# Kernel tuning notes

Hardware: AMD Instinct MI355X
Metric: run time of the kernel (lower is better)

Reference implementation:

```python
import jax, jax.numpy as jnp
import numpy as np

LN_EPS = 1e-5


def _layer_norm(x, scale, bias):
    mu = jnp.mean(x, axis=-1, keepdims=True)
    var = jnp.mean(jnp.square(x - mu), axis=-1, keepdims=True)
    return (x - mu) * jax.lax.rsqrt(var + LN_EPS) * scale + bias


def setup_inputs() -> dict:
    key = jax.random.key(0)
    B, N, C_Z, C_H = 1, 512, 128, 128
    ks = jax.random.split(key, 8)
    s = 1.0 / np.sqrt(C_Z)
    inp = {
        "z": jax.random.normal(ks[0], (B, N, N, C_Z), dtype=jnp.float32),
        "mask": jnp.ones((B, N, N), dtype=jnp.float32),
        # gated / plain projections from c_z -> c_hidden
        "w_a_p": jax.random.normal(ks[1], (C_Z, C_H), dtype=jnp.float32) * s,
        "b_a_p": jnp.zeros((C_H,), dtype=jnp.float32),
        "w_a_g": jnp.zeros((C_Z, C_H), dtype=jnp.float32),  # gating init: zeros, bias ones
        "b_a_g": jnp.ones((C_H,), dtype=jnp.float32),
        "w_b_p": jax.random.normal(ks[2], (C_Z, C_H), dtype=jnp.float32) * s,
        "b_b_p": jnp.zeros((C_H,), dtype=jnp.float32),
        "w_b_g": jnp.zeros((C_Z, C_H), dtype=jnp.float32),
        "b_b_g": jnp.ones((C_H,), dtype=jnp.float32),
        # output gate c_z -> c_z (gating init)
        "w_g": jnp.zeros((C_Z, C_Z), dtype=jnp.float32),
        "b_g": jnp.ones((C_Z,), dtype=jnp.float32),
        # final projection c_hidden -> c_z ('final' init: zeros; use small randn for a nontrivial test)
        "w_z": jax.random.normal(ks[3], (C_H, C_Z), dtype=jnp.float32) * (1.0 / np.sqrt(C_H)),
        "b_z": jnp.zeros((C_Z,), dtype=jnp.float32),
        "ln_in_scale": jnp.ones((C_Z,), dtype=jnp.float32),
        "ln_in_bias": jnp.zeros((C_Z,), dtype=jnp.float32),
        "ln_out_scale": jnp.ones((C_H,), dtype=jnp.float32),
        "ln_out_bias": jnp.zeros((C_H,), dtype=jnp.float32),
    }
    return inp


def reference(z, mask, w_a_p, b_a_p, w_a_g, b_a_g, w_b_p, b_b_p, w_b_g, b_b_g,
              w_g, b_g, w_z, b_z, ln_in_scale, ln_in_bias, ln_out_scale, ln_out_bias):
    # tmu_type == 'outgoing'
    z = _layer_norm(z, ln_in_scale, ln_in_bias)          # [B,N,N,Cz]
    m = mask[..., None]                                   # [B,N,N,1]
    a = jax.nn.sigmoid(z @ w_a_g + b_a_g) * m * (z @ w_a_p + b_a_p)  # [B,N,N,Ch]
    b = jax.nn.sigmoid(z @ w_b_g + b_b_g) * m * (z @ w_b_p + b_b_p)  # [B,N,N,Ch]
    # outgoing: p[b,i,j,c] = sum_k a[b,i,k,c] * b[b,j,k,c]
    x = jnp.einsum("bikc,bjkc->bijc", a, b)              # [B,N,N,Ch]
    x = _layer_norm(x, ln_out_scale, ln_out_bias)
    x = x @ w_z + b_z                                    # [B,N,N,Cz]
    g = jax.nn.sigmoid(z @ w_g + b_g)                    # [B,N,N,Cz]
    return x * g
```

## Files before the change

### kernel.cpp

```cpp
#include <hip/hip_runtime.h>

typedef __attribute__((ext_vector_type(8))) short short8;
typedef __attribute__((ext_vector_type(4))) short short4v;
typedef __attribute__((ext_vector_type(4))) float float4v;

#define NDIM 512
#define NN (NDIM*NDIM)
#define CD 128

__device__ __forceinline__ unsigned short f2b(float f) {
  union { float f; unsigned u; } v; v.f = f;
  unsigned r = v.u + 0x7FFFu + ((v.u >> 16) & 1u);
  return (unsigned short)(r >> 16);
}
__device__ __forceinline__ float b2f(unsigned short h) {
  union { unsigned u; float f; } v; v.u = ((unsigned)h) << 16; return v.f;
}
__device__ __forceinline__ float sigmoidf_(float x) {
  return __fdividef(1.f, 1.f + __expf(-x));
}
__device__ __forceinline__ unsigned pk2(float a, float b) {
  unsigned r;
  asm("v_cvt_pk_bf16_f32 %0, %1, %2" : "=v"(r) : "v"(a), "v"(b));
  return r;
}
__device__ __forceinline__ float4v mfma16(short8 a, short8 b, float4v c) {
  return __builtin_amdgcn_mfma_f32_16x16x32_bf16(a, b, c, 0, 0, 0);
}
__device__ __forceinline__ void gl_lds16(const short* g, short* l) {
  __builtin_amdgcn_global_load_lds(
      (const __attribute__((address_space(1))) unsigned int*)g,
      (__attribute__((address_space(3))) unsigned int*)l, 16, 0, 0);
}

__device__ __forceinline__ short8 fragr(const short* buf, int row, int j) {
  return *(const short8*)(buf + row * 128 + ((j ^ (row & 15)) << 3));
}
__device__ __forceinline__ void stg_w(short* buf, int row, int ku, unsigned v) {
  *(unsigned*)&buf[row * 128 + ((((ku >> 2) ^ (row & 15)) << 3) + ((ku & 3) << 1))] = v;
}
__device__ __forceinline__ void stg_w2(short* buf, int row, int ku, unsigned v0, unsigned v1) {
  unsigned long long v = (unsigned long long)v0 | ((unsigned long long)v1 << 32);
  *(unsigned long long*)&buf[row * 128 + ((((ku >> 2) ^ (row & 15)) << 3) + ((ku & 3) << 1))] = v;
}

__global__ __launch_bounds__(256) void kPrepW(
    const float* __restrict__ w0, const float* __restrict__ w1,
    const float* __restrict__ w2, const float* __restrict__ w3,
    const float* __restrict__ w4, short* __restrict__ wt)
{
  const int wi = blockIdx.y;
  const float* W = wi==0 ? w0 : wi==1 ? w1 : wi==2 ? w2 : wi==3 ? w3 : w4;
  const int e = blockIdx.x * 256 + threadIdx.x;
  const int k = e >> 7, n = e & 127;
  wt[wi * 16384 + n * 128 + k] = (short)f2b(W[k * CD + n]);
}

__global__ __launch_bounds__(512, 4) void kProj(
    const float* __restrict__ z, const float* __restrict__ mask,
    const short* __restrict__ wT,
    const float* __restrict__ b_a_p, const float* __restrict__ b_a_g,
    const float* __restrict__ b_b_p, const float* __restrict__ b_b_g,
    const float* __restrict__ b_g,
    const float* __restrict__ ln_s, const float* __restrict__ ln_b,
    short* __restrict__ a_t, short* __restrict__ b_t, short* __restrict__ g_out)
{
  __shared__ short zln[128 * 128];
  __shared__ short sS[64 * 128];
  __shared__ short wA[64 * 128];
  __shared__ short wB[64 * 128];
  const int t = threadIdx.x;
  const int bid = blockIdx.x;
  const int sw = (bid & 7) * 512 + (bid >> 3);
  const int ch_half = sw & 1;
  const int r0 = (sw >> 1) * 128;
  const int choff = ch_half * 64;
  const int w = t >> 6, l = t & 63, lr = l & 15, lg = l >> 4;
  const int wr = w * 16;

#define STAGE2H(BUF, SLOT) do { _Pragma("unroll") for (int i_=0;i_<2;++i_) {        \
    int U_ = i_*512 + t; int row_ = U_ >> 4, u_ = U_ & 15;                          \
    gl_lds16(wT + (SLOT)*16384 + (choff + row_)*128 + ((u_^(row_&15))<<3), (BUF)+U_*8); } } while(0)

  STAGE2H(wA, 1);
  STAGE2H(wB, 0);

  {
    const int row = t >> 2, q = t & 3;
    const float* zp = z + (size_t)(r0 + row) * CD + q * 32;
    float x[32];
#pragma unroll
    for (int i = 0; i < 8; ++i) {
      float4v v = *(const float4v*)(zp + i * 4);
#pragma unroll
      for (int e = 0; e < 4; ++e) x[i*4+e] = v[e];
    }
    float s = 0.f;
#pragma unroll
    for (int i = 0; i < 32; ++i) s += x[i];
    s += __shfl_xor(s, 1, 64);
    s += __shfl_xor(s, 2, 64);
    const float mu = s * (1.f/128.f);
    float vs = 0.f;
#pragma unroll
    for (int i = 0; i < 32; ++i) { float d = x[i]-mu; vs += d*d; }
    vs += __shfl_xor(vs, 1, 64);
    vs += __shfl_xor(vs, 2, 64);
    const float rstd = rsqrtf(vs * (1.f/128.f) + 1e-5f);
#pragma unroll
    for (int i = 0; i < 32; i += 4) {
      int c = q*32 + i;
      float y0 = (x[i]  -mu)*rstd*ln_s[c]   + ln_b[c];
      float y1 = (x[i+1]-mu)*rstd*ln_s[c+1] + ln_b[c+1];
      float y2 = (x[i+2]-mu)*rstd*ln_s[c+2] + ln_b[c+2];
      float y3 = (x[i+3]-mu)*rstd*ln_s[c+3] + ln_b[c+3];
      int addr = row*128 + (((c>>3) ^ (row & 15)) << 3) + (c & 7);
      unsigned long long pv = (unsigned long long)pk2(y0, y1)
                            | ((unsigned long long)pk2(y2, y3) << 32);
      *(unsigned long long*)(&zln[addr]) = pv;
    }
  }

  float bga[4], bpa[4], bgb[4], bpb[4];
#pragma unroll
  for (int cf = 0; cf < 4; ++cf) {
    int ci = choff + cf*16 + lr;
    bga[cf] = b_a_g[ci]; bpa[cf] = b_a_p[ci];
    bgb[cf] = b_b_g[ci]; bpb[cf] = b_b_p[ci];
  }
  float mrow[4];
#pragma unroll
  for (int jj = 0; jj < 4; ++jj) mrow[jj] = mask[r0 + wr + lg*4 + jj];

  __syncthreads();

  short8 af[4];
#pragma unroll
  for (int ks = 0; ks < 4; ++ks)
    af[ks] = fragr(zln, wr + lr, ks*4 + lg);

  float4v accG[4], accB[4];
  float sg[4][4];

#define ZERO4(A) do { _Pragma("unroll") for (int c_=0;c_<4;++c_) A[c_] = (float4v){0.f,0.f,0.f,0.f}; } while(0)

#define WP(ACC, BUF) do { ZERO4(ACC);                                      \
  _Pragma("unroll") for (int ks_=0; ks_<4; ++ks_)                          \
    _Pragma("unroll") for (int cf_=0; cf_<4; ++cf_) {                      \
      short8 wf_ = fragr(BUF, cf_*16 + lr, ks_*4 + lg);                    \
      ACC[cf_] = mfma16(af[ks_], wf_, ACC[cf_]);                           \
    } } while(0)

#define SIG4(BG) do { _Pragma("unroll") for (int cf_=0;cf_<4;++cf_)        \
    _Pragma("unroll") for (int j_=0;j_<4;++j_)                             \
      sg[cf_][j_] = sigmoidf_(accG[cf_][j_] + BG[cf_]) * mrow[j_]; } while(0)

#define PKAB(BP) do { _Pragma("unroll") for (int cf_=0;cf_<4;++cf_) {      \
    float v0_ = sg[cf_][0]*(accB[cf_][0]+BP[cf_]);                         \
    float v1_ = sg[cf_][1]*(accB[cf_][1]+BP[cf_]);                         \
    float v2_ = sg[cf_][2]*(accB[cf_][2]+BP[cf_]);                         \
    float v3_ = sg[cf_][3]*(accB[cf_][3]+BP[cf_]);                         \
    int ch_ = cf_*16 + lr, ku_ = (wr >> 1) + lg*2;                         \
    stg_w2(sS, ch_, ku_, pk2(v0_, v1_), pk2(v2_, v3_)); } } while(0)

#define STORE64A(DST) do { int ch_ = t >> 3;                               \
  _Pragma("unroll") for (int i_=0;i_<2;++i_) {                             \
    int cL_ = (t & 7)*2 + i_;                                              \
    *(short8*)(DST + (size_t)(choff + ch_)*NN + r0 + cL_*8) = fragr(sS, ch_, cL_); \
  } } while(0)

  WP(accG, wA);
  WP(accB, wB);
  SIG4(bga);
  PKAB(bpa);
  __syncthreads();

  STAGE2H(wA, 3);
  STAGE2H(wB, 2);
  STAGE2H(zln, 4);
  STORE64A(a_t);
  __syncthreads();

  WP(accG, wA);
  WP(accB, wB);
  float4v accG2[4];
  ZERO4(accG2);
#pragma unroll
  for (int ks = 0; ks < 4; ++ks)
#pragma unroll
    for (int cf = 0; cf < 4; ++cf) {
      short8 wf = fragr(zln, cf*16 + lr, ks*4 + lg);
      accG2[cf] = mfma16(wf, af[ks], accG2[cf]);
    }
  SIG4(bgb);
  PKAB(bpb);
  __syncthreads();

  STORE64A(b_t);
#pragma unroll
  for (int cf = 0; cf < 4; ++cf) {
    float4v bgv = *(const float4v*)(b_g + choff + cf*16 + lg*4);
    float v0 = sigmoidf_(accG2[cf][0] + bgv[0]);
    float v1 = sigmoidf_(accG2[cf][1] + bgv[1]);
    float v2 = sigmoidf_(accG2[cf][2] + bgv[2]);
    float v3 = sigmoidf_(accG2[cf][3] + bgv[3]);
    int row = wr + lr, ku = cf*8 + lg*2;
    stg_w2(zln, row, ku, pk2(v0, v1), pk2(v2, v3));
  }
  __syncthreads();

  {
    int row = t >> 2;
#pragma unroll
    for (int i = 0; i < 2; ++i) {
      int cL = (t & 3)*2 + i;
      *(short8*)(g_out + (size_t)(r0 + row)*CD + choff + cL*8) = fragr(zln, row, cL);
    }
  }
}

__global__ __launch_bounds__(256, 2) void kEinsum(const short* __restrict__ a_t,
                                                  const short* __restrict__ b_t,
                                                  short* __restrict__ x_t)
{
  __shared__ short As[2][128 * 64];
  __shared__ short Bs[2][128 * 64];
  const int t = threadIdx.x;
  const int d = blockIdx.x;
  const int c = (d & 7) * 16 + (d >> 7);
  const int tile = (d >> 3) & 15;
  const int i0 = (tile >> 2) * 128;
  const int j0 = (tile & 3) * 128;
  const size_t abase = (size_t)c * NN;
  const int w = t >> 6, l = t & 63, lr = l & 15, lg = l >> 4;
  const int wr = w >> 1, wc = w & 1;

  const short* gA[4]; const short* gB[4]; int ldsU[4];
#pragma unroll
  for (int q = 0; q < 4; ++q) {
    int U = q * 256 + t;
    int row = U >> 3, u = U & 7;
    int swz = ((u ^ (row & 7)) << 3);
    gA[q] = a_t + abase + (size_t)(i0 + row) * NDIM + swz;
    gB[q] = b_t + abase + (size_t)(j0 + row) * NDIM + swz;
    ldsU[q] = U * 8;
  }

#define STAGE_E(buf, k0) do { _Pragma("unroll") for (int q_=0;q_<4;++q_) { \
    gl_lds16(gA[q_] + (k0), &As[buf][ldsU[q_]]);                           \
    gl_lds16(gB[q_] + (k0), &Bs[buf][ldsU[q_]]); } } while(0)

  float4v acc[4][4];
#pragma unroll
  for (int m = 0; m < 4; ++m)
#pragma unroll
    for (int n = 0; n < 4; ++n) acc[m][n] = (float4v){0.f,0.f,0.f,0.f};

  STAGE_E(0, 0);
  STAGE_E(1, 64);
#pragma unroll
  for (int it = 0; it < 8; ++it) {
    if (it < 7) asm volatile("s_waitcnt vmcnt(8)" ::: "memory");
    else        asm volatile("s_waitcnt vmcnt(0)" ::: "memory");
    __builtin_amdgcn_sched_barrier(0);
    __builtin_amdgcn_s_barrier();
    const short* Ab = &As[it & 1][0];
    const short* Bb = &Bs[it & 1][0];
    short8 afr[4][2], bfr[4][2];
#pragma unroll
    for (int m = 0; m < 4; ++m)
#pragma unroll
      for (int ks = 0; ks < 2; ++ks) {
        int row = wr*64 + m*16 + lr, j = ks*4 + lg;
        afr[m][ks] = *(const short8*)(Ab + row*64 + ((j ^ (row & 7)) << 3));
      }
#pragma unroll
    for (int n = 0; n < 4; ++n)
#pragma unroll
      for (int ks = 0; ks < 2; ++ks) {
        int row = wc*64 + n*16 + lr, j = ks*4 + lg;
        bfr[n][ks] = *(const short8*)(Bb + row*64 + ((j ^ (row & 7)) << 3));
      }
    __builtin_amdgcn_s_setprio(1);
#pragma unroll
    for (int ks = 0; ks < 2; ++ks)
#pragma unroll
      for (int m = 0; m < 4; ++m)
#pragma unroll
        for (int n = 0; n < 4; ++n)
          acc[m][n] = mfma16(bfr[n][ks], afr[m][ks], acc[m][n]);
    __builtin_amdgcn_s_setprio(0);
    __builtin_amdgcn_s_barrier();
    __builtin_amdgcn_sched_barrier(0);
    if (it < 6) STAGE_E(it & 1, (it + 2) * 64);
  }
  short* Xs = &As[0][0];
#pragma unroll
  for (int m = 0; m < 4; ++m)
#pragma unroll
    for (int n = 0; n < 4; ++n) {
      int il = wr*64 + m*16 + lr;
      int ku = wc*32 + n*8 + lg*2;
      stg_w2(Xs, il, ku, pk2(acc[m][n][0], acc[m][n][1]),
                         pk2(acc[m][n][2], acc[m][n][3]));
    }
  __syncthreads();
#pragma unroll
  for (int i = 0; i < 8; ++i) {
    int il = t >> 1, cL = (t & 1)*8 + i;
    *(short8*)(x_t + abase + (size_t)(i0 + il)*NDIM + j0 + cL*8) = fragr(Xs, il, cL);
  }
}

__global__ __launch_bounds__(1024, 4) void kOut(
    const short* __restrict__ x_t, const short* __restrict__ g_in,
    const float* __restrict__ w_z, const float* __restrict__ b_z,
    const float* __restrict__ ln_s, const float* __restrict__ ln_b,
    float* __restrict__ out)
{
  __shared__ short xs[128 * 128];
  __shared__ short xln[128 * 128];
  __shared__ short sW[128 * 128];
  const int t = threadIdx.x;
  const int r0 = blockIdx.x * 128;
  const int w = t >> 6, l = t & 63, lr = l & 15, lg = l >> 4;
  const int rowb = (w >> 1) * 16;
  const int hc = (w & 1) * 64;

  short8 gv[2];
#pragma unroll
  for (int v = 0; v < 2; ++v) {
    int V = v*1024 + t; int row = V >> 4, u = V & 15;
    gv[v] = *(const short8*)(g_in + (size_t)(r0 + row) * CD + u * 8);
  }
#pragma unroll
  for (int v = 0; v < 2; ++v) {
    int U = v*1024 + t; int cc = U >> 4, u = U & 15;
    gl_lds16(x_t + (size_t)cc * NN + r0 + ((u ^ ((cc >> 3) & 15)) << 3), xs + U*8);
  }
#pragma unroll
  for (int i = 0; i < 2; ++i) {
    int flat = i*1024 + t;
    int kp = flat >> 5, k = kp * 2, n4 = (flat & 31) * 4;
    float4v va = *(const float4v*)(w_z + (size_t)k * CD + n4);
    float4v vb = *(const float4v*)(w_z + (size_t)(k + 1) * CD + n4);
#pragma unroll
    for (int j = 0; j < 4; ++j) {
      int row = n4 + j;
      int addr = row * 128 + (((k >> 3) ^ (row & 15)) << 3) + (k & 7);
      *(unsigned*)(&sW[addr]) = pk2(va[j], vb[j]);
    }
  }
  __syncthreads();
  {
    const int r = t >> 3, q = t & 7;
    float x[16];
#pragma unroll
    for (int i = 0; i < 16; ++i) {
      int c = q*16 + i;
      x[i] = b2f((unsigned short)xs[c*128 + (((r >> 3) ^ ((c >> 3) & 15)) << 3) + (r & 7)]);
    }
    float s = 0.f;
#pragma unroll
    for (int i = 0; i < 16; ++i) s += x[i];
    s += __shfl_xor(s, 1, 64);
    s += __shfl_xor(s, 2, 64);
    s += __shfl_xor(s, 4, 64);
    const float mu = s * (1.f/128.f);
    float vs = 0.f;
#pragma unroll
    for (int i = 0; i < 16; ++i) { float d = x[i]-mu; vs += d*d; }
    vs += __shfl_xor(vs, 1, 64);
    vs += __shfl_xor(vs, 2, 64);
    vs += __shfl_xor(vs, 4, 64);
    const float rstd = rsqrtf(vs * (1.f/128.f) + 1e-5f);
#pragma unroll
    for (int i = 0; i < 16; i += 4) {
      int c = q*16 + i;
      float y0 = (x[i]  -mu)*rstd*ln_s[c]   + ln_b[c];
      float y1 = (x[i+1]-mu)*rstd*ln_s[c+1] + ln_b[c+1];
      float y2 = (x[i+2]-mu)*rstd*ln_s[c+2] + ln_b[c+2];
      float y3 = (x[i+3]-mu)*rstd*ln_s[c+3] + ln_b[c+3];
      int addr = r*128 + (((c>>3) ^ (r & 15)) << 3) + (c & 7);
      unsigned long long pv = (unsigned long long)pk2(y0, y1)
                            | ((unsigned long long)pk2(y2, y3) << 32);
      *(unsigned long long*)(&xln[addr]) = pv;
    }
  }
  __syncthreads();
  short* sG = xs;
#pragma unroll
  for (int v = 0; v < 2; ++v) {
    int V = v*1024 + t; int row = V >> 4, u = V & 15;
    *(short8*)(sG + row*128 + ((u ^ (row & 15)) << 3)) = gv[v];
  }
  short8 af[4];
#pragma unroll
  for (int ks = 0; ks < 4; ++ks)
    af[ks] = fragr(xln, rowb + lr, ks*4 + lg);
  float4v acc[4];
#pragma unroll
  for (int cf = 0; cf < 4; ++cf) acc[cf] = (float4v){0.f,0.f,0.f,0.f};
#pragma unroll
  for (int ks = 0; ks < 4; ++ks)
#pragma unroll
    for (int cf = 0; cf < 4; ++cf) {
      short8 wf = fragr(sW, hc + cf*16 + lr, ks*4 + lg);
      acc[cf] = mfma16(af[ks], wf, acc[cf]);
    }
  float bz[4];
#pragma unroll
  for (int cf = 0; cf < 4; ++cf) bz[cf] = b_z[hc + cf*16 + lr];
  __syncthreads();
#pragma unroll
  for (int cf = 0; cf < 4; ++cf) {
    int ch = hc + cf*16 + lr;
#pragma unroll
    for (int jj = 0; jj < 4; ++jj) {
      int row = rowb + lg*4 + jj;
      float gvv = b2f((unsigned short)sG[row*128 + (((ch>>3) ^ (row & 15)) << 3) + (ch & 7)]);
      out[(size_t)(r0 + row) * CD + ch] = (acc[cf][jj] + bz[cf]) * gvv;
    }
  }
}

extern "C" void kernel_launch(void* const* d_in, const int* in_sizes, int n_in,
                              void* d_out, int out_size, void* d_ws, size_t ws_size,
                              hipStream_t stream) {
  (void)in_sizes; (void)n_in; (void)out_size; (void)ws_size;
  const float* z     = (const float*)d_in[0];
  const float* mask  = (const float*)d_in[1];
  const float* w_a_p = (const float*)d_in[2];
  const float* b_a_p = (const float*)d_in[3];
  const float* w_a_g = (const float*)d_in[4];
  const float* b_a_g = (const float*)d_in[5];
  const float* w_b_p = (const float*)d_in[6];
  const float* b_b_p = (const float*)d_in[7];
  const float* w_b_g = (const float*)d_in[8];
  const float* b_b_g = (const float*)d_in[9];
  const float* w_g   = (const float*)d_in[10];
  const float* b_g   = (const float*)d_in[11];
  const float* w_z   = (const float*)d_in[12];
  const float* b_z   = (const float*)d_in[13];
  const float* ln_i_s = (const float*)d_in[14];
  const float* ln_i_b = (const float*)d_in[15];
  const float* ln_o_s = (const float*)d_in[16];
  const float* ln_o_b = (const float*)d_in[17];

  short* a_t = (short*)d_ws;
  short* b_t = a_t + (size_t)CD*NN;
  short* g_s = b_t + (size_t)CD*NN;
  short* x_t = g_s + (size_t)CD*NN;
  short* wT  = x_t;

  hipLaunchKernelGGL(kPrepW, dim3(64, 5), dim3(256), 0, stream,
                     w_a_p, w_a_g, w_b_p, w_b_g, w_g, wT);
  hipLaunchKernelGGL(kProj, dim3(4096), dim3(512), 0, stream,
                     z, mask, wT, b_a_p, b_a_g, b_b_p, b_b_g, b_g,
                     ln_i_s, ln_i_b, a_t, b_t, g_s);
  hipLaunchKernelGGL(kEinsum, dim3(2048), dim3(256), 0, stream, a_t, b_t, x_t);
  hipLaunchKernelGGL(kOut, dim3(NN/128), dim3(1024), 0, stream,
                     x_t, g_s, w_z, b_z, ln_o_s, ln_o_b, (float*)d_out);
}
```

Baseline: 313.0 us.

## Enlarge einsum block tile to 128x256 with 8 waves

The batched einsum kernel now computes a 128x256 output tile per block with 512 threads instead of 128x128 with 256 threads, halving the grid. Each A tile loaded from global memory is reused across twice as many output columns, which cuts global and LDS-fill traffic for A per output element. The cost is doubled LDS for the B buffers (about 96KB per block), which may limit occupancy to one block per CU, and an adjusted vmcnt wait count and epilogue that stages output through the B buffer.

```diff
diff --git a/kernel.cpp b/kernel.cpp
--- a/kernel.cpp
+++ b/kernel.cpp
@@ -219,36 +219,44 @@
   }
 }
 
-__global__ __launch_bounds__(256, 2) void kEinsum(const short* __restrict__ a_t,
+__global__ __launch_bounds__(512, 2) void kEinsum(const short* __restrict__ a_t,
                                                   const short* __restrict__ b_t,
                                                   short* __restrict__ x_t)
 {
   __shared__ short As[2][128 * 64];
-  __shared__ short Bs[2][128 * 64];
+  __shared__ short Bs[2][256 * 64];
   const int t = threadIdx.x;
   const int d = blockIdx.x;
-  const int c = (d & 7) * 16 + (d >> 7);
-  const int tile = (d >> 3) & 15;
-  const int i0 = (tile >> 2) * 128;
-  const int j0 = (tile & 3) * 128;
+  const int c = (d & 7) * 16 + (d >> 6);
+  const int tile = (d >> 3) & 7;
+  const int i0 = (tile >> 1) * 128;
+  const int j0 = (tile & 1) * 256;
   const size_t abase = (size_t)c * NN;
   const int w = t >> 6, l = t & 63, lr = l & 15, lg = l >> 4;
-  const int wr = w >> 1, wc = w & 1;
-
-  const short* gA[4]; const short* gB[4]; int ldsU[4];
+  const int wr = w >> 2, wc = w & 3;
+
+  const short* gA[2]; int ldsA[2];
+#pragma unroll
+  for (int q = 0; q < 2; ++q) {
+    int U = q * 512 + t;
+    int row = U >> 3, u = U & 7;
+    gA[q] = a_t + abase + (size_t)(i0 + row) * NDIM + ((u ^ (row & 7)) << 3);
+    ldsA[q] = U * 8;
+  }
+  const short* gB[4]; int ldsB[4];
 #pragma unroll
   for (int q = 0; q < 4; ++q) {
-    int U = q * 256 + t;
+    int U = q * 512 + t;
     int row = U >> 3, u = U & 7;
-    int swz = ((u ^ (row & 7)) << 3);
-    gA[q] = a_t + abase + (size_t)(i0 + row) * NDIM + swz;
-    gB[q] = b_t + abase + (size_t)(j0 + row) * NDIM + swz;
-    ldsU[q] = U * 8;
-  }
-
-#define STAGE_E(buf, k0) do { _Pragma("unroll") for (int q_=0;q_<4;++q_) { \
-    gl_lds16(gA[q_] + (k0), &As[buf][ldsU[q_]]);                           \
-    gl_lds16(gB[q_] + (k0), &Bs[buf][ldsU[q_]]); } } while(0)
+    gB[q] = b_t + abase + (size_t)(j0 + row) * NDIM + ((u ^ (row & 7)) << 3);
+    ldsB[q] = U * 8;
+  }
+
+#define STAGE_E3(buf, k0) do {                                             \
+    _Pragma("unroll") for (int q_=0;q_<2;++q_)                             \
+      gl_lds16(gA[q_] + (k0), &As[buf][ldsA[q_]]);                         \
+    _Pragma("unroll") for (int q_=0;q_<4;++q_)                             \
+      gl_lds16(gB[q_] + (k0), &Bs[buf][ldsB[q_]]); } while(0)
 
   float4v acc[4][4];
 #pragma unroll
@@ -256,11 +264,11 @@
 #pragma unroll
     for (int n = 0; n < 4; ++n) acc[m][n] = (float4v){0.f,0.f,0.f,0.f};
 
-  STAGE_E(0, 0);
-  STAGE_E(1, 64);
+  STAGE_E3(0, 0);
+  STAGE_E3(1, 64);
 #pragma unroll
   for (int it = 0; it < 8; ++it) {
-    if (it < 7) asm volatile("s_waitcnt vmcnt(8)" ::: "memory");
+    if (it < 7) asm volatile("s_waitcnt vmcnt(6)" ::: "memory");
     else        asm volatile("s_waitcnt vmcnt(0)" ::: "memory");
     __builtin_amdgcn_sched_barrier(0);
     __builtin_amdgcn_s_barrier();
@@ -292,24 +300,28 @@
     __builtin_amdgcn_s_setprio(0);
     __builtin_amdgcn_s_barrier();
     __builtin_amdgcn_sched_barrier(0);
-    if (it < 6) STAGE_E(it & 1, (it + 2) * 64);
-  }
-  short* Xs = &As[0][0];
+    if (it < 6) STAGE_E3(it & 1, (it + 2) * 64);
+  }
+  short* Xs = &Bs[0][0];
 #pragma unroll
   for (int m = 0; m < 4; ++m)
 #pragma unroll
     for (int n = 0; n < 4; ++n) {
       int il = wr*64 + m*16 + lr;
-      int ku = wc*32 + n*8 + lg*2;
-      stg_w2(Xs, il, ku, pk2(acc[m][n][0], acc[m][n][1]),
-                         pk2(acc[m][n][2], acc[m][n][3]));
-    }
-  __syncthreads();
-#pragma unroll
-  for (int i = 0; i < 8; ++i) {
-    int il = t >> 1, cL = (t & 1)*8 + i;
-    *(short8*)(x_t + abase + (size_t)(i0 + il)*NDIM + j0 + cL*8) = fragr(Xs, il, cL);
-  }
+      int h = wc >> 1;
+      int ku = (wc & 1)*32 + n*8 + lg*2;
+      stg_w2(Xs + h*16384, il, ku, pk2(acc[m][n][0], acc[m][n][1]),
+                                   pk2(acc[m][n][2], acc[m][n][3]));
+    }
+  __syncthreads();
+#pragma unroll
+  for (int h = 0; h < 2; ++h)
+#pragma unroll
+    for (int i = 0; i < 4; ++i) {
+      int il = t >> 2, cL = (t & 3)*4 + i;
+      *(short8*)(x_t + abase + (size_t)(i0 + il)*NDIM + j0 + h*128 + cL*8)
+          = fragr(Xs + h*16384, il, cL);
+    }
 }
 
 __global__ __launch_bounds__(1024, 4) void kOut(
@@ -458,7 +470,7 @@
   hipLaunchKernelGGL(kProj, dim3(4096), dim3(512), 0, stream,
                      z, mask, wT, b_a_p, b_a_g, b_b_p, b_b_g, b_g,
                      ln_i_s, ln_i_b, a_t, b_t, g_s);
-  hipLaunchKernelGGL(kEinsum, dim3(2048), dim3(256), 0, stream, a_t, b_t, x_t);
+  hipLaunchKernelGGL(kEinsum, dim3(1024), dim3(512), 0, stream, a_t, b_t, x_t);
   hipLaunchKernelGGL(kOut, dim3(NN/128), dim3(1024), 0, stream,
                      x_t, g_s, w_z, b_z, ln_o_s, ln_o_b, (float*)d_out);
 }
```

New measurement: 314.3 us. About the same (+0.4%).
